# Performance work log

Measured on AMD Instinct MI355X. Metric: run time of the kernel, lower is better.

## Reference

```python
import math
import jax, jax.numpy as jnp
import numpy as np

B, S, HID = 2, 2048, 1024
NH, DQ, DV = 16, 64, 64

def _alibi_bias(n_heads, maxlen):
    # standard ALiBi slopes: 2^(-8*(h+1)/n_heads)
    slopes = jnp.asarray([2.0 ** (-8.0 * (h + 1) / n_heads) for h in range(n_heads)], dtype=jnp.float32)
    pos = jnp.arange(maxlen, dtype=jnp.float32)
    rel = pos[None, :] - pos[:, None]              # [i, j] = j - i  (<= 0 on causal part)
    return slopes[:, None, None] * rel[None]       # [n_heads, maxlen, maxlen]

def setup_inputs() -> dict:
    key = jax.random.key(0)
    ks = jax.random.split(key, 6)
    scale = 0.02
    return {
        "hidden_states": jax.random.normal(ks[0], (B, S, HID), dtype=jnp.float32),
        "attention_mask": jnp.ones((B, S), dtype=jnp.int32),
        "Wq": jax.random.normal(ks[1], (HID, NH * DQ), dtype=jnp.float32) * scale,
        "Wk": jax.random.normal(ks[2], (HID, NH * DQ), dtype=jnp.float32) * scale,
        "Wv": jax.random.normal(ks[3], (HID, NH * DV), dtype=jnp.float32) * scale,
        "Wo": jax.random.normal(ks[4], (NH * DV, HID), dtype=jnp.float32) * scale,
        "bo": jnp.zeros((HID,), dtype=jnp.float32),
        "alibi": _alibi_bias(NH, S),
    }

def reference(hidden_states, attention_mask, Wq, Wk, Wv, Wo, bo, alibi):
    N, t, _ = hidden_states.shape
    # QKV projections (no bias), split into heads: [N, H, t, d]
    q = (hidden_states @ Wq).reshape(N, t, NH, DQ).transpose(0, 2, 1, 3)
    k = (hidden_states @ Wk).reshape(N, t, NH, DQ).transpose(0, 2, 1, 3)
    v = (hidden_states @ Wv).reshape(N, t, NH, DV).transpose(0, 2, 1, 3)
    # raw scores, then ALiBi added BEFORE the 1/sqrt(d) scaling (as in source)
    scores = jnp.einsum("bhid,bhjd->bhij", q, k)
    scores = scores + alibi[None, :, :t, :t]
    scores = scores / math.sqrt(DQ)
    # grok tanh softcap at 30
    scores = 30.0 * jnp.tanh(scores / 30.0)
    # causal + padding masks
    causal = jnp.tril(jnp.ones((t, t), dtype=bool))
    scores = jnp.where(causal[None, None], scores, -jnp.inf)
    pad = (attention_mask != 0)[:, None, None, :]  # [N,1,1,T]
    scores = jnp.where(pad, scores, -jnp.inf)
    probs = jax.nn.softmax(scores, axis=-1)        # dropout p=0.0 (eval)
    ctx = jnp.einsum("bhij,bhjd->bhid", probs, v)
    ctx = ctx.transpose(0, 2, 1, 3).reshape(N, t, NH * DV)
    out = ctx @ Wo + bo
    return out
```

## Files before the change

kernel.cpp:

```cpp
#include <hip/hip_runtime.h>
#include <stdint.h>

#define BB 2
#define SS 2048
#define HID 1024
#define NHEAD 16
#define DHEAD 64
#define MTOT (BB*SS)

typedef float  f32x4  __attribute__((ext_vector_type(4)));
typedef short  s16x8  __attribute__((ext_vector_type(8)));
typedef unsigned short u16x4 __attribute__((ext_vector_type(4)));

#define LOG2E 1.4426950408889634f

__device__ __forceinline__ unsigned short f2bf(float x){
  union { float f; unsigned u; } v; v.f = x;
  unsigned r = v.u + 0x7fffu + ((v.u >> 16) & 1u);
  return (unsigned short)(r >> 16);
}
__device__ __forceinline__ float bf2f(unsigned short h){
  union { unsigned u; float f; } v; v.u = ((unsigned)h) << 16; return v.f;
}

__device__ __forceinline__ void gl2lds16(const unsigned short* g, unsigned short* l){
  __builtin_amdgcn_global_load_lds((const __attribute__((address_space(1))) void*)g,
                                   (__attribute__((address_space(3))) void*)l, 16, 0, 0);
}

__global__ __launch_bounds__(256) void k_convert_x(const float* __restrict__ x,
                                                   unsigned short* __restrict__ xb){
  int i = blockIdx.x * 256 + threadIdx.x;
  const float4* xp = (const float4*)x;
  float4 v = xp[i];
  u16x4 o; o.x = f2bf(v.x); o.y = f2bf(v.y); o.z = f2bf(v.z); o.w = f2bf(v.w);
  ((u16x4*)xb)[i] = o;
}

__global__ __launch_bounds__(256) void k_convert_w(const float* __restrict__ Wq,
                                                   const float* __restrict__ Wk,
                                                   const float* __restrict__ Wv,
                                                   const float* __restrict__ Wo,
                                                   unsigned short* __restrict__ Wt,
                                                   unsigned short* __restrict__ Wot){
  __shared__ float tile[64][65];
  int z = blockIdx.z;
  const float* src = (z==0) ? Wq : (z==1) ? Wk : (z==2) ? Wv : Wo;
  unsigned short* dst = (z < 3) ? (Wt + z * HID * HID) : Wot;
  int n0 = blockIdx.x * 64, k0 = blockIdx.y * 64;
  int t = threadIdx.x, tx = t & 63, ty = t >> 6;
  #pragma unroll
  for (int i = 0; i < 16; i++){
    int kl = ty + i*4;
    tile[kl][tx] = src[(k0 + kl) * HID + n0 + tx];
  }
  __syncthreads();
  #pragma unroll
  for (int i = 0; i < 16; i++){
    int nl = ty + i*4;
    dst[(n0 + nl) * HID + k0 + tx] = f2bf(tile[tx][nl]);
  }
}

__global__ __launch_bounds__(256) void k_gemm_qkv(const unsigned short* __restrict__ A,
                                                  const unsigned short* __restrict__ Bt,
                                                  unsigned short* __restrict__ Qb,
                                                  unsigned short* __restrict__ Kb,
                                                  unsigned short* __restrict__ Vb){
  __shared__ __align__(16) unsigned short As[128*32];
  __shared__ __align__(16) unsigned short Bs[128*32];
  int t = threadIdx.x;
  int L = t & 63, w = t >> 6;
  int q = L >> 4, c = L & 15;
  int m0 = blockIdx.x * 128, n0 = blockIdx.y * 128;
  int wr = w >> 1, wc = w & 1;
  f32x4 acc[4][4];
  #pragma unroll
  for (int i = 0; i < 4; i++)
    #pragma unroll
    for (int j = 0; j < 4; j++) acc[i][j] = (f32x4){0.f,0.f,0.f,0.f};

  for (int kb = 0; kb < 32; kb++){
    __syncthreads();
    #pragma unroll
    for (int i = 0; i < 2; i++){
      int p = t + i*256;
      int row = p >> 2, cp = p & 3;
      gl2lds16(A  + (m0 + row) * HID + kb*32 + cp*8, As + p*8);
      gl2lds16(Bt + (n0 + row) * HID + kb*32 + cp*8, Bs + p*8);
    }
    __syncthreads();
    s16x8 af[4], bf[4];
    #pragma unroll
    for (int i = 0; i < 4; i++){
      int m = wr*64 + i*16 + c;
      af[i] = *(const s16x8*)(As + m*32 + q*8);
      int n = wc*64 + i*16 + c;
      bf[i] = *(const s16x8*)(Bs + n*32 + q*8);
    }
    #pragma unroll
    for (int i = 0; i < 4; i++)
      #pragma unroll
      for (int j = 0; j < 4; j++)
        acc[i][j] = __builtin_amdgcn_mfma_f32_16x16x32_bf16(af[i], bf[j], acc[i][j], 0, 0, 0);
  }

  int wsel = n0 >> 10;
  unsigned short* dst = (wsel==0) ? Qb : (wsel==1) ? Kb : Vb;
  float scale = (wsel==0) ? 0.125f : 1.0f;
  #pragma unroll
  for (int i = 0; i < 4; i++){
    #pragma unroll
    for (int j = 0; j < 4; j++){
      int m_l = wr*64 + i*16 + q*4;
      int nw  = (n0 + wc*64 + j*16 + c) & 1023;
      #pragma unroll
      for (int r = 0; r < 4; r++)
        dst[(m0 + m_l + r) * HID + nw] = f2bf(acc[i][j][r] * scale);
    }
  }
}

__global__ __launch_bounds__(256) void k_transpose_v(const unsigned short* __restrict__ Vb,
                                                     unsigned short* __restrict__ Vt){
  __shared__ unsigned tile[64][33];
  int st = blockIdx.x, bh = blockIdx.y;
  int b = bh >> 4, h = bh & 15;
  int t = threadIdx.x;
  int lr = t >> 4, lc = t & 15;
  #pragma unroll
  for (int i = 0; i < 4; i++){
    int sl = lr + i*16;
    u16x4 v = *(const u16x4*)(Vb + (size_t)(b*SS + st*64 + sl) * HID + h*DHEAD + lc*4);
    tile[sl][lc*2]     = (unsigned)v.x | ((unsigned)v.y << 16);
    tile[sl][lc*2 + 1] = (unsigned)v.z | ((unsigned)v.w << 16);
  }
  __syncthreads();
  #pragma unroll
  for (int i = 0; i < 4; i++){
    int dl = lr + i*16;
    int sh = (dl & 1) * 16, dw = dl >> 1;
    u16x4 o;
    o.x = (unsigned short)(tile[lc*4 + 0][dw] >> sh);
    o.y = (unsigned short)(tile[lc*4 + 1][dw] >> sh);
    o.z = (unsigned short)(tile[lc*4 + 2][dw] >> sh);
    o.w = (unsigned short)(tile[lc*4 + 3][dw] >> sh);
    *(u16x4*)(Vt + (size_t)(bh*DHEAD + dl) * SS + st*64 + lc*4) = o;
  }
}

__global__ __launch_bounds__(256) void k_attn(const unsigned short* __restrict__ Qb,
                                              const unsigned short* __restrict__ Kb,
                                              const unsigned short* __restrict__ Vt,
                                              const int* __restrict__ amask,
                                              unsigned short* __restrict__ NumBf,
                                              float* __restrict__ Lsum,
                                              float* __restrict__ Part2,
                                              float* __restrict__ L2){
  __shared__ __align__(16) unsigned short UQ[4*16*72];
  __shared__ __align__(16) unsigned short Ks[64*64];
  __shared__ __align__(16) unsigned short Vs[64*64];

  int t = threadIdx.x;
  int L = t & 63, w = t >> 6;
  int q = L >> 4, c = L & 15;
  int x = blockIdx.x;
  int bh = blockIdx.y;
  int b = bh >> 4, h = bh & 15;

  int qt, jt0, jt1, chunk1;
  if (x < 32){
    qt = 31 - (x >> 1);
    int h0 = (qt + 1) >> 1;
    chunk1 = x & 1;
    jt0 = chunk1 ? h0 : 0;
    jt1 = chunk1 ? (qt + 1) : h0;
  } else {
    qt = 47 - x;
    jt0 = 0; jt1 = qt + 1; chunk1 = 0;
  }
  int i0 = qt * 64;

  int hp = h + 1;
  float slope = (hp & 1) ? 0.70710678118654752f : 1.0f;
  slope = ldexpf(slope, -((hp >> 1) + 3));

  #pragma unroll
  for (int i = 0; i < 2; i++){
    int p = t + i*256; int row = p >> 3, cp = p & 7; int gc = cp ^ (row & 7);
    gl2lds16(Qb + (size_t)(b*SS + i0 + row) * HID + h*DHEAD + gc*8, UQ + p*8);
  }
  __syncthreads();
  s16x8 qf0, qf1;
  {
    int m = w*16 + c;
    qf0 = *(const s16x8*)(UQ + m*64 + ((0 + q) ^ (m & 7)) * 8);
    qf1 = *(const s16x8*)(UQ + m*64 + ((4 + q) ^ (m & 7)) * 8);
  }

  float si[4];
  #pragma unroll
  for (int r = 0; r < 4; r++) si[r] = slope * (float)(i0 + w*16 + q*4 + r);

  f32x4 cacc[4];
  #pragma unroll
  for (int i = 0; i < 4; i++) cacc[i] = (f32x4){0.f,0.f,0.f,0.f};
  float lrow[4] = {0.f,0.f,0.f,0.f};

  const float C1 = 86.5617024533378f;
  const float C2 = 0.0961796693925976f;

  for (int jt = jt0; jt < jt1; jt++){
    int j0 = jt * 64;
    __syncthreads();
    #pragma unroll
    for (int i = 0; i < 2; i++){
      int p = t + i*256; int row = p >> 3, cp = p & 7; int gc = cp ^ (row & 7);
      gl2lds16(Kb + (size_t)(b*SS + j0 + row) * HID + h*DHEAD + gc*8, Ks + p*8);
      gl2lds16(Vt + (size_t)(bh*DHEAD + row) * SS + j0 + gc*8, Vs + p*8);
    }
    __syncthreads();

    f32x4 sacc[4];
    #pragma unroll
    for (int ct = 0; ct < 4; ct++){
      int n = ct*16 + c;
      s16x8 kf0 = *(const s16x8*)(Ks + n*64 + ((0 + q) ^ (n & 7)) * 8);
      s16x8 kf1 = *(const s16x8*)(Ks + n*64 + ((4 + q) ^ (n & 7)) * 8);
      f32x4 z = (f32x4){0.f,0.f,0.f,0.f};
      z = __builtin_amdgcn_mfma_f32_16x16x32_bf16(qf0, kf0, z, 0, 0, 0);
      z = __builtin_amdgcn_mfma_f32_16x16x32_bf16(qf1, kf1, z, 0, 0, 0);
      sacc[ct] = z;
    }

    float p_[4][4];
    #pragma unroll
    for (int ct = 0; ct < 4; ct++){
      int jg = j0 + ct*16 + c;
      float padf = (amask[b*SS + jg] != 0) ? 1.0f : 0.0f;
      float sjg = slope * (float)jg;
      #pragma unroll
      for (int r = 0; r < 4; r++){
        float s = sacc[ct][r] + (sjg - si[r]);
        float e2 = exp2f(s * C2);
        float pv = exp2f(-C1 * __builtin_amdgcn_rcpf(e2 + 1.0f));
        p_[ct][r] = pv * padf;
      }
    }
    if (jt == qt){
      #pragma unroll
      for (int ct = 0; ct < 4; ct++){
        int jg = j0 + ct*16 + c;
        #pragma unroll
        for (int r = 0; r < 4; r++){
          int ig = i0 + w*16 + q*4 + r;
          if (jg > ig) p_[ct][r] = 0.0f;
        }
      }
    }
    #pragma unroll
    for (int ct = 0; ct < 4; ct++)
      #pragma unroll
      for (int r = 0; r < 4; r++) lrow[r] += p_[ct][r];

    unsigned short* pw = UQ + w * (16*72);
    #pragma unroll
    for (int ct = 0; ct < 4; ct++)
      #pragma unroll
      for (int r = 0; r < 4; r++)
        pw[(q*4 + r)*72 + ct*16 + c] = f2bf(p_[ct][r]);

    s16x8 pf0 = *(const s16x8*)(pw + c*72 + q*8);
    s16x8 pf1 = *(const s16x8*)(pw + c*72 + 32 + q*8);
    #pragma unroll
    for (int nt = 0; nt < 4; nt++){
      int d = nt*16 + c;
      s16x8 vf0 = *(const s16x8*)(Vs + d*64 + ((0 + q) ^ (d & 7)) * 8);
      s16x8 vf1 = *(const s16x8*)(Vs + d*64 + ((4 + q) ^ (d & 7)) * 8);
      cacc[nt] = __builtin_amdgcn_mfma_f32_16x16x32_bf16(pf0, vf0, cacc[nt], 0, 0, 0);
      cacc[nt] = __builtin_amdgcn_mfma_f32_16x16x32_bf16(pf1, vf1, cacc[nt], 0, 0, 0);
    }
  }

  float lred[4];
  #pragma unroll
  for (int r = 0; r < 4; r++){
    float l = lrow[r];
    l += __shfl_xor(l, 1, 64);
    l += __shfl_xor(l, 2, 64);
    l += __shfl_xor(l, 4, 64);
    l += __shfl_xor(l, 8, 64);
    lred[r] = l;
  }

  if (!chunk1){
    #pragma unroll
    for (int nt = 0; nt < 4; nt++){
      int d = nt*16 + c;
      #pragma unroll
      for (int r = 0; r < 4; r++){
        int ig = i0 + w*16 + q*4 + r;
        NumBf[(size_t)(b*SS + ig) * HID + h*DHEAD + d] = f2bf(cacc[nt][r]);
      }
    }
    if (c == 0){
      #pragma unroll
      for (int r = 0; r < 4; r++)
        Lsum[bh*SS + i0 + w*16 + q*4 + r] = lred[r];
    }
  } else {
    int slot = bh*16 + (qt - 16);
    float* pn = Part2 + (size_t)slot * 64 * 64;
    #pragma unroll
    for (int nt = 0; nt < 4; nt++){
      int d = nt*16 + c;
      #pragma unroll
      for (int r = 0; r < 4; r++){
        int row = w*16 + q*4 + r;
        pn[row*64 + d] = cacc[nt][r];
      }
    }
    if (c == 0){
      #pragma unroll
      for (int r = 0; r < 4; r++)
        L2[slot*64 + w*16 + q*4 + r] = lred[r];
    }
  }
}

__global__ __launch_bounds__(256) void k_combine(unsigned short* __restrict__ NumBf,
                                                 const float* __restrict__ Lsum,
                                                 const float* __restrict__ Part2,
                                                 const float* __restrict__ L2){
  int idx = blockIdx.x * 256 + threadIdx.x;
  int tok = idx >> 8;
  int hd4 = (idx & 255) * 4;
  int h = hd4 >> 6, d0 = hd4 & 63;
  int b = tok >> 11, i = tok & 2047;
  int bh = b*16 + h, qt = i >> 6;
  u16x4 nv = *(u16x4*)(NumBf + (size_t)tok * HID + hd4);
  float n0 = bf2f(nv.x), n1 = bf2f(nv.y), n2 = bf2f(nv.z), n3 = bf2f(nv.w);
  float l = Lsum[bh*SS + i];
  if (qt >= 16){
    int slot = bh*16 + (qt - 16);
    const float* pn = Part2 + ((size_t)slot * 64 + (i & 63)) * 64 + d0;
    n0 += pn[0]; n1 += pn[1]; n2 += pn[2]; n3 += pn[3];
    l += L2[slot*64 + (i & 63)];
  }
  float rl = __builtin_amdgcn_rcpf(l);
  u16x4 o;
  o.x = f2bf(n0*rl); o.y = f2bf(n1*rl); o.z = f2bf(n2*rl); o.w = f2bf(n3*rl);
  *(u16x4*)(NumBf + (size_t)tok * HID + hd4) = o;
}

__global__ __launch_bounds__(256) void k_gemm_out(const unsigned short* __restrict__ A,
                                                  const unsigned short* __restrict__ Bt,
                                                  float* __restrict__ out,
                                                  const float* __restrict__ bo){
  __shared__ __align__(16) unsigned short As[128*32];
  __shared__ __align__(16) unsigned short Bs[128*32];
  int t = threadIdx.x;
  int L = t & 63, w = t >> 6;
  int q = L >> 4, c = L & 15;
  int m0 = blockIdx.x * 128, n0 = blockIdx.y * 128;
  int wr = w >> 1, wc = w & 1;
  f32x4 acc[4][4];
  #pragma unroll
  for (int i = 0; i < 4; i++)
    #pragma unroll
    for (int j = 0; j < 4; j++) acc[i][j] = (f32x4){0.f,0.f,0.f,0.f};

  for (int kb = 0; kb < 32; kb++){
    __syncthreads();
    #pragma unroll
    for (int i = 0; i < 2; i++){
      int p = t + i*256;
      int row = p >> 2, cp = p & 3;
      gl2lds16(A  + (m0 + row) * HID + kb*32 + cp*8, As + p*8);
      gl2lds16(Bt + (n0 + row) * HID + kb*32 + cp*8, Bs + p*8);
    }
    __syncthreads();
    s16x8 af[4], bf[4];
    #pragma unroll
    for (int i = 0; i < 4; i++){
      int m = wr*64 + i*16 + c;
      af[i] = *(const s16x8*)(As + m*32 + q*8);
      int n = wc*64 + i*16 + c;
      bf[i] = *(const s16x8*)(Bs + n*32 + q*8);
    }
    #pragma unroll
    for (int i = 0; i < 4; i++)
      #pragma unroll
      for (int j = 0; j < 4; j++)
        acc[i][j] = __builtin_amdgcn_mfma_f32_16x16x32_bf16(af[i], bf[j], acc[i][j], 0, 0, 0);
  }

  #pragma unroll
  for (int j = 0; j < 4; j++){
    int n = n0 + wc*64 + j*16 + c;
    float bv = bo[n];
    #pragma unroll
    for (int i = 0; i < 4; i++){
      int m = m0 + wr*64 + i*16 + q*4;
      #pragma unroll
      for (int r = 0; r < 4; r++)
        out[(size_t)(m + r) * HID + n] = acc[i][j][r] + bv;
    }
  }
}

extern "C" void kernel_launch(void* const* d_in, const int* in_sizes, int n_in,
                              void* d_out, int out_size, void* d_ws, size_t ws_size,
                              hipStream_t stream){
  const float* hs    = (const float*)d_in[0];
  const int*   amask = (const int*)  d_in[1];
  const float* Wq    = (const float*)d_in[2];
  const float* Wk    = (const float*)d_in[3];
  const float* Wv    = (const float*)d_in[4];
  const float* Wo    = (const float*)d_in[5];
  const float* bo    = (const float*)d_in[6];
  float* out = (float*)d_out;

  char* ws = (char*)d_ws;
  unsigned short* Xb  = (unsigned short*)(ws);
  unsigned short* Wt  = (unsigned short*)(ws + (8u  << 20));
  unsigned short* Wot = (unsigned short*)(ws + (14u << 20));
  unsigned short* Qb  = (unsigned short*)(ws + (16u << 20));
  unsigned short* Kb  = (unsigned short*)(ws + (24u << 20));
  unsigned short* Vt  = (unsigned short*)(ws + (32u << 20));
  unsigned short* Ctx = (unsigned short*)(ws + (40u << 20));
  float* Part2 = (float*)(ws);
  float* L2    = (float*)(ws + (8u << 20));
  float* Lsum  = (float*)(ws + (8u << 20) + (512u << 10));
  unsigned short* Vb = Ctx;

  hipLaunchKernelGGL(k_convert_x,  dim3(MTOT*HID/4/256), dim3(256), 0, stream, hs, Xb);
  hipLaunchKernelGGL(k_convert_w,  dim3(16,16,4), dim3(256), 0, stream, Wq, Wk, Wv, Wo, Wt, Wot);
  hipLaunchKernelGGL(k_gemm_qkv,   dim3(32,24),   dim3(256), 0, stream, Xb, Wt, Qb, Kb, Vb);
  hipLaunchKernelGGL(k_transpose_v,dim3(32,32),   dim3(256), 0, stream, Vb, Vt);
  hipLaunchKernelGGL(k_attn,       dim3(48,32),   dim3(256), 0, stream, Qb, Kb, Vt, amask,
                                   Ctx, Lsum, Part2, L2);
  hipLaunchKernelGGL(k_combine,    dim3(MTOT*HID/4/256), dim3(256), 0, stream, Ctx, Lsum, Part2, L2);
  hipLaunchKernelGGL(k_gemm_out,   dim3(32,8),    dim3(256), 0, stream, Ctx, Wot, out, bo);
}
```

Before: 471.9 us.

## Fuse conversion kernels, transpose V in QKV GEMM epilogue, shrink out-GEMM tile

The two fp32-to-bf16 conversion kernels become one launch that switches on block index. The V transpose moves into the QKV GEMM epilogue through shared memory, which removes a separate kernel and a round trip of V through global memory. The output GEMM tile shrinks from 128x128 to 128x64, doubling the grid to 512 blocks so the GPU is better filled, at the cost of less data reuse per block.

```diff
diff --git a/kernel.cpp b/kernel.cpp
--- a/kernel.cpp
+++ b/kernel.cpp
@@ -28,27 +28,31 @@
                                    (__attribute__((address_space(3))) void*)l, 16, 0, 0);
 }
 
-__global__ __launch_bounds__(256) void k_convert_x(const float* __restrict__ x,
-                                                   unsigned short* __restrict__ xb){
-  int i = blockIdx.x * 256 + threadIdx.x;
-  const float4* xp = (const float4*)x;
-  float4 v = xp[i];
-  u16x4 o; o.x = f2bf(v.x); o.y = f2bf(v.y); o.z = f2bf(v.z); o.w = f2bf(v.w);
-  ((u16x4*)xb)[i] = o;
-}
-
-__global__ __launch_bounds__(256) void k_convert_w(const float* __restrict__ Wq,
-                                                   const float* __restrict__ Wk,
-                                                   const float* __restrict__ Wv,
-                                                   const float* __restrict__ Wo,
-                                                   unsigned short* __restrict__ Wt,
-                                                   unsigned short* __restrict__ Wot){
+__global__ __launch_bounds__(256) void k_convert(const float* __restrict__ x,
+                                                 const float* __restrict__ Wq,
+                                                 const float* __restrict__ Wk,
+                                                 const float* __restrict__ Wv,
+                                                 const float* __restrict__ Wo,
+                                                 unsigned short* __restrict__ xb,
+                                                 unsigned short* __restrict__ Wt,
+                                                 unsigned short* __restrict__ Wot){
   __shared__ float tile[64][65];
-  int z = blockIdx.z;
+  int bx = blockIdx.x;
+  int t = threadIdx.x;
+  if (bx < 4096){
+    int i = bx * 256 + t;
+    const float4* xp = (const float4*)x;
+    float4 v = xp[i];
+    u16x4 o; o.x = f2bf(v.x); o.y = f2bf(v.y); o.z = f2bf(v.z); o.w = f2bf(v.w);
+    ((u16x4*)xb)[i] = o;
+    return;
+  }
+  int idx = bx - 4096;
+  int z = idx >> 8, ky = (idx >> 4) & 15, nx = idx & 15;
   const float* src = (z==0) ? Wq : (z==1) ? Wk : (z==2) ? Wv : Wo;
   unsigned short* dst = (z < 3) ? (Wt + z * HID * HID) : Wot;
-  int n0 = blockIdx.x * 64, k0 = blockIdx.y * 64;
-  int t = threadIdx.x, tx = t & 63, ty = t >> 6;
+  int n0 = nx * 64, k0 = ky * 64;
+  int tx = t & 63, ty = t >> 6;
   #pragma unroll
   for (int i = 0; i < 16; i++){
     int kl = ty + i*4;
@@ -66,9 +70,10 @@
                                                   const unsigned short* __restrict__ Bt,
                                                   unsigned short* __restrict__ Qb,
                                                   unsigned short* __restrict__ Kb,
-                                                  unsigned short* __restrict__ Vb){
-  __shared__ __align__(16) unsigned short As[128*32];
-  __shared__ __align__(16) unsigned short Bs[128*32];
+                                                  unsigned short* __restrict__ Vt){
+  __shared__ __align__(16) unsigned short smem[128*64];
+  unsigned short* As = smem;
+  unsigned short* Bs = smem + 128*32;
   int t = threadIdx.x;
   int L = t & 63, w = t >> 6;
   int q = L >> 4, c = L & 15;
@@ -106,46 +111,52 @@
   }
 
   int wsel = n0 >> 10;
-  unsigned short* dst = (wsel==0) ? Qb : (wsel==1) ? Kb : Vb;
-  float scale = (wsel==0) ? 0.125f : 1.0f;
-  #pragma unroll
-  for (int i = 0; i < 4; i++){
-    #pragma unroll
-    for (int j = 0; j < 4; j++){
-      int m_l = wr*64 + i*16 + q*4;
-      int nw  = (n0 + wc*64 + j*16 + c) & 1023;
-      #pragma unroll
-      for (int r = 0; r < 4; r++)
-        dst[(m0 + m_l + r) * HID + nw] = f2bf(acc[i][j][r] * scale);
-    }
-  }
-}
-
-__global__ __launch_bounds__(256) void k_transpose_v(const unsigned short* __restrict__ Vb,
-                                                     unsigned short* __restrict__ Vt){
-  __shared__ unsigned tile[64][33];
-  int st = blockIdx.x, bh = blockIdx.y;
-  int b = bh >> 4, h = bh & 15;
-  int t = threadIdx.x;
-  int lr = t >> 4, lc = t & 15;
-  #pragma unroll
-  for (int i = 0; i < 4; i++){
-    int sl = lr + i*16;
-    u16x4 v = *(const u16x4*)(Vb + (size_t)(b*SS + st*64 + sl) * HID + h*DHEAD + lc*4);
-    tile[sl][lc*2]     = (unsigned)v.x | ((unsigned)v.y << 16);
-    tile[sl][lc*2 + 1] = (unsigned)v.z | ((unsigned)v.w << 16);
-  }
-  __syncthreads();
-  #pragma unroll
-  for (int i = 0; i < 4; i++){
-    int dl = lr + i*16;
-    int sh = (dl & 1) * 16, dw = dl >> 1;
-    u16x4 o;
-    o.x = (unsigned short)(tile[lc*4 + 0][dw] >> sh);
-    o.y = (unsigned short)(tile[lc*4 + 1][dw] >> sh);
-    o.z = (unsigned short)(tile[lc*4 + 2][dw] >> sh);
-    o.w = (unsigned short)(tile[lc*4 + 3][dw] >> sh);
-    *(u16x4*)(Vt + (size_t)(bh*DHEAD + dl) * SS + st*64 + lc*4) = o;
+  if (wsel < 2){
+    unsigned short* dst = (wsel==0) ? Qb : Kb;
+    float scale = (wsel==0) ? 0.125f : 1.0f;
+    #pragma unroll
+    for (int i = 0; i < 4; i++){
+      #pragma unroll
+      for (int j = 0; j < 4; j++){
+        int m_l = wr*64 + i*16 + q*4;
+        int nw  = (n0 + wc*64 + j*16 + c) & 1023;
+        #pragma unroll
+        for (int r = 0; r < 4; r++)
+          dst[(m0 + m_l + r) * HID + nw] = f2bf(acc[i][j][r] * scale);
+      }
+    }
+  } else {
+    int nwb = n0 & 1023;
+    int b   = m0 >> 11;
+    int sloc= m0 & 2047;
+    #pragma unroll
+    for (int half = 0; half < 2; half++){
+      __syncthreads();
+      if (wc == half){
+        #pragma unroll
+        for (int i = 0; i < 4; i++){
+          #pragma unroll
+          for (int j = 0; j < 4; j++){
+            int hd64 = j*16 + c;
+            int m_l  = wr*64 + i*16 + q*4;
+            u16x4 pk;
+            pk.x = f2bf(acc[i][j][0]); pk.y = f2bf(acc[i][j][1]);
+            pk.z = f2bf(acc[i][j][2]); pk.w = f2bf(acc[i][j][3]);
+            *(u16x4*)(smem + hd64*128 + m_l) = pk;
+          }
+        }
+      }
+      __syncthreads();
+      int hgl = (nwb >> 6) + half;
+      size_t base = ((size_t)((b*NHEAD + hgl)*DHEAD)) * SS + sloc;
+      #pragma unroll
+      for (int it = 0; it < 4; it++){
+        int u = t + it*256;
+        int d = u >> 4, sc = u & 15;
+        s16x8 v = *(const s16x8*)(smem + d*128 + sc*8);
+        *(s16x8*)(Vt + base + (size_t)d * SS + sc*8) = v;
+      }
+    }
   }
 }
 
@@ -358,15 +369,14 @@
                                                   float* __restrict__ out,
                                                   const float* __restrict__ bo){
   __shared__ __align__(16) unsigned short As[128*32];
-  __shared__ __align__(16) unsigned short Bs[128*32];
+  __shared__ __align__(16) unsigned short Bs[64*32];
   int t = threadIdx.x;
   int L = t & 63, w = t >> 6;
   int q = L >> 4, c = L & 15;
-  int m0 = blockIdx.x * 128, n0 = blockIdx.y * 128;
-  int wr = w >> 1, wc = w & 1;
-  f32x4 acc[4][4];
-  #pragma unroll
-  for (int i = 0; i < 4; i++)
+  int m0 = blockIdx.x * 128, n0 = blockIdx.y * 64;
+  f32x4 acc[2][4];
+  #pragma unroll
+  for (int i = 0; i < 2; i++)
     #pragma unroll
     for (int j = 0; j < 4; j++) acc[i][j] = (f32x4){0.f,0.f,0.f,0.f};
 
@@ -376,20 +386,26 @@
     for (int i = 0; i < 2; i++){
       int p = t + i*256;
       int row = p >> 2, cp = p & 3;
-      gl2lds16(A  + (m0 + row) * HID + kb*32 + cp*8, As + p*8);
-      gl2lds16(Bt + (n0 + row) * HID + kb*32 + cp*8, Bs + p*8);
-    }
-    __syncthreads();
-    s16x8 af[4], bf[4];
-    #pragma unroll
-    for (int i = 0; i < 4; i++){
-      int m = wr*64 + i*16 + c;
+      gl2lds16(A + (m0 + row) * HID + kb*32 + cp*8, As + p*8);
+    }
+    {
+      int row = t >> 2, cp = t & 3;
+      gl2lds16(Bt + (n0 + row) * HID + kb*32 + cp*8, Bs + t*8);
+    }
+    __syncthreads();
+    s16x8 af[2], bf[4];
+    #pragma unroll
+    for (int i = 0; i < 2; i++){
+      int m = w*32 + i*16 + c;
       af[i] = *(const s16x8*)(As + m*32 + q*8);
-      int n = wc*64 + i*16 + c;
-      bf[i] = *(const s16x8*)(Bs + n*32 + q*8);
-    }
-    #pragma unroll
-    for (int i = 0; i < 4; i++)
+    }
+    #pragma unroll
+    for (int j = 0; j < 4; j++){
+      int n = j*16 + c;
+      bf[j] = *(const s16x8*)(Bs + n*32 + q*8);
+    }
+    #pragma unroll
+    for (int i = 0; i < 2; i++)
       #pragma unroll
       for (int j = 0; j < 4; j++)
         acc[i][j] = __builtin_amdgcn_mfma_f32_16x16x32_bf16(af[i], bf[j], acc[i][j], 0, 0, 0);
@@ -397,11 +413,11 @@
 
   #pragma unroll
   for (int j = 0; j < 4; j++){
-    int n = n0 + wc*64 + j*16 + c;
+    int n = n0 + j*16 + c;
     float bv = bo[n];
     #pragma unroll
-    for (int i = 0; i < 4; i++){
-      int m = m0 + wr*64 + i*16 + q*4;
+    for (int i = 0; i < 2; i++){
+      int m = m0 + w*32 + i*16 + q*4;
       #pragma unroll
       for (int r = 0; r < 4; r++)
         out[(size_t)(m + r) * HID + n] = acc[i][j][r] + bv;
@@ -432,14 +448,12 @@
   float* Part2 = (float*)(ws);
   float* L2    = (float*)(ws + (8u << 20));
   float* Lsum  = (float*)(ws + (8u << 20) + (512u << 10));
-  unsigned short* Vb = Ctx;
-
-  hipLaunchKernelGGL(k_convert_x,  dim3(MTOT*HID/4/256), dim3(256), 0, stream, hs, Xb);
-  hipLaunchKernelGGL(k_convert_w,  dim3(16,16,4), dim3(256), 0, stream, Wq, Wk, Wv, Wo, Wt, Wot);
-  hipLaunchKernelGGL(k_gemm_qkv,   dim3(32,24),   dim3(256), 0, stream, Xb, Wt, Qb, Kb, Vb);
-  hipLaunchKernelGGL(k_transpose_v,dim3(32,32),   dim3(256), 0, stream, Vb, Vt);
-  hipLaunchKernelGGL(k_attn,       dim3(48,32),   dim3(256), 0, stream, Qb, Kb, Vt, amask,
-                                   Ctx, Lsum, Part2, L2);
-  hipLaunchKernelGGL(k_combine,    dim3(MTOT*HID/4/256), dim3(256), 0, stream, Ctx, Lsum, Part2, L2);
-  hipLaunchKernelGGL(k_gemm_out,   dim3(32,8),    dim3(256), 0, stream, Ctx, Wot, out, bo);
-}
+
+  hipLaunchKernelGGL(k_convert,  dim3(4096 + 1024), dim3(256), 0, stream,
+                     hs, Wq, Wk, Wv, Wo, Xb, Wt, Wot);
+  hipLaunchKernelGGL(k_gemm_qkv, dim3(32,24), dim3(256), 0, stream, Xb, Wt, Qb, Kb, Vt);
+  hipLaunchKernelGGL(k_attn,     dim3(48,32), dim3(256), 0, stream, Qb, Kb, Vt, amask,
+                                 Ctx, Lsum, Part2, L2);
+  hipLaunchKernelGGL(k_combine,  dim3(MTOT*HID/4/256), dim3(256), 0, stream, Ctx, Lsum, Part2, L2);
+  hipLaunchKernelGGL(k_gemm_out, dim3(32,16), dim3(256), 0, stream, Ctx, Wot, out, bo);
+}
```

Result: slower. 491.5 us (+4.1%).
